# Kernel optimization log

Measured on AMD Instinct MI355X. Metric: run time of the kernel, lower is better.

The kernel has to match this reference:

```python
import jax, jax.numpy as jnp
import numpy as np

N_NODES = 50000
N_EDGES = 1600000
HID = 128
N_LAYERS = 4
EPS = 1e-5
NEG_SLOPE = 0.2


def setup_inputs() -> dict:
    key = jax.random.key(0)
    ks = jax.random.split(key, 10)
    x = jax.random.normal(ks[0], (N_NODES, HID), dtype=jnp.float32)
    edge_index = jax.random.randint(ks[1], (2, N_EDGES), 0, N_NODES, dtype=jnp.int64)
    edge_label_index = jax.random.randint(ks[2], (2, 8192), 0, N_NODES, dtype=jnp.int64)
    s = 1.0 / np.sqrt(HID)
    Wl = jax.random.uniform(ks[3], (N_LAYERS, HID, HID), jnp.float32, -s, s)
    Wr = jax.random.uniform(ks[4], (N_LAYERS, HID, HID), jnp.float32, -s, s)
    att = jax.random.uniform(ks[5], (N_LAYERS, HID), jnp.float32, -s, s)
    bias = jnp.zeros((N_LAYERS, HID), jnp.float32)
    gamma = jnp.ones((N_LAYERS, HID), jnp.float32)
    beta = jnp.zeros((N_LAYERS, HID), jnp.float32)
    return {"x": x, "edge_index": edge_index, "edge_label_index": edge_label_index,
            "Wl": Wl, "Wr": Wr, "att": att, "bias": bias, "gamma": gamma, "beta": beta}


def _gatv2_layer(x, Wl, Wr, a, b, src, dst):
    # GATv2Conv, single head: e_ij = a^T LeakyReLU(W_l x_j + W_r x_i)
    xl = x @ Wl                       # [N, H] source transform (also the message)
    xr = x @ Wr                       # [N, H] target transform
    e = jax.nn.leaky_relu(xl[src] + xr[dst], NEG_SLOPE) @ a   # [E]
    emax = jax.ops.segment_max(e, dst, num_segments=N_NODES)  # per-target max
    ew = jnp.exp(e - emax[dst])
    denom = jax.ops.segment_sum(ew, dst, num_segments=N_NODES)
    alpha = ew / denom[dst]
    out = jax.ops.segment_sum(alpha[:, None] * xl[src], dst, num_segments=N_NODES)
    return out + b


def _batchnorm(x, g, b):
    mu = jnp.mean(x, axis=0)
    var = jnp.mean(jnp.square(x - mu), axis=0)  # biased var (training mode)
    return (x - mu) * jax.lax.rsqrt(var + EPS) * g + b


def _embedding(x, edge_index, Wl, Wr, att, bias, gamma, beta):
    loops = jnp.arange(N_NODES, dtype=edge_index.dtype)
    src = jnp.concatenate([edge_index[0], loops])
    dst = jnp.concatenate([edge_index[1], loops])
    resw = 1.0 / (N_LAYERS + 1)  # alpha buffer, all entries equal
    h = x
    out = None
    for i in range(N_LAYERS):
        h = _gatv2_layer(h, Wl[i], Wr[i], att[i], bias[i], src, dst)
        h = _batchnorm(h, gamma[i], beta[i])
        out = h * resw if out is None else out + h * resw
    return out


def reference(x, edge_index, edge_label_index, Wl, Wr, att, bias, gamma, beta):
    out = _embedding(x, edge_index, Wl, Wr, att, bias, gamma, beta)
    return (out[edge_label_index[0]] * out[edge_label_index[1]]).sum(axis=-1)
```

## Files before the change

### kernel.cpp

```cpp
#include <hip/hip_runtime.h>
#include <hip/hip_bf16.h>
#include <hip/hip_fp16.h>

#define N_NODES 50000
#define N_EDGES 1600000
#define ET (N_EDGES + N_NODES)
#define HID 128
#define N_LAYERS 4
#define EPS 1e-5f
#define NEG 0.2f
#define RB 256
#define NBUCK 782
#define BCHUNK 8192
#define LOG2E 1.44269504088896f

typedef __attribute__((ext_vector_type(8))) short s16x8;
typedef __attribute__((ext_vector_type(8))) __bf16 bfx8;
typedef __attribute__((ext_vector_type(4))) float fx4;
typedef __attribute__((ext_vector_type(2))) _Float16 f16x2;

__device__ __forceinline__ unsigned int packbf2(float a, float b) {
    unsigned int ua = __float_as_uint(a);
    ua = (ua + 0x7fffu + ((ua >> 16) & 1u)) >> 16;
    unsigned int ub = __float_as_uint(b);
    ub = (ub + 0x7fffu + ((ub >> 16) & 1u)) & 0xffff0000u;
    return (ua & 0xffffu) | ub;
}
__device__ __forceinline__ unsigned short bf16r(float a) {
    unsigned int ua = __float_as_uint(a);
    return (unsigned short)((ua + 0x7fffu + ((ua >> 16) & 1u)) >> 16);
}
__device__ __forceinline__ unsigned int packh2(float a, float b) {
    return __builtin_bit_cast(unsigned int, __builtin_amdgcn_cvt_pkrtz(a, b));
}
__device__ __forceinline__ f16x2 packh2v(float a, float b) {
    return __builtin_bit_cast(f16x2, __builtin_amdgcn_cvt_pkrtz(a, b));
}
__device__ __forceinline__ float2 unpackh2(unsigned int u) {
    f16x2 h = __builtin_bit_cast(f16x2, u);
    return make_float2((float)h.x, (float)h.y);
}

__global__ void bucket_zero_kernel(int* __restrict__ gcnt) {
    int i = blockIdx.x * 256 + threadIdx.x;
    if (i < NBUCK) gcnt[i] = 0;
}

__global__ __launch_bounds__(256) void bucket_hist_kernel(const int* __restrict__ ei,
                                                          int* __restrict__ gcnt) {
    __shared__ int h[NBUCK];
    for (int i = threadIdx.x; i < NBUCK; i += 256) h[i] = 0;
    __syncthreads();
    int base = blockIdx.x * BCHUNK;
    int lim = min(base + BCHUNK, ET);
    for (int i = base + threadIdx.x; i < lim; i += 256) {
        int dst = (i < N_EDGES) ? ei[N_EDGES + i] : i - N_EDGES;
        atomicAdd(&h[dst >> 6], 1);
    }
    __syncthreads();
    for (int i = threadIdx.x; i < NBUCK; i += 256)
        if (h[i]) atomicAdd(&gcnt[i], h[i]);
}

__global__ void bucket_scan_kernel(const int* __restrict__ gcnt, int* __restrict__ bbase,
                                   int* __restrict__ bcur, int* __restrict__ rowptr) {
    __shared__ int sh[1024];
    int tid = threadIdx.x;
    int v = (tid < NBUCK) ? gcnt[tid] : 0;
    sh[tid] = v;
    __syncthreads();
    for (int off = 1; off < 1024; off <<= 1) {
        int t = (tid >= off) ? sh[tid - off] : 0;
        __syncthreads();
        sh[tid] += t;
        __syncthreads();
    }
    if (tid < NBUCK) {
        int ex = sh[tid] - v;
        bbase[tid] = ex;
        bcur[tid] = ex;
    }
    if (tid == NBUCK - 1) bbase[NBUCK] = sh[tid];
    if (tid == 0) rowptr[N_NODES] = ET;
}

__global__ __launch_bounds__(256) void bucket_scatter_kernel(const int* __restrict__ ei,
                                                             int* __restrict__ bcur,
                                                             unsigned int* __restrict__ pairs) {
    __shared__ int h[NBUCK];
    __shared__ int rbase[NBUCK];
    for (int i = threadIdx.x; i < NBUCK; i += 256) h[i] = 0;
    __syncthreads();
    int base = blockIdx.x * BCHUNK;
    int lim = min(base + BCHUNK, ET);
    for (int i = base + threadIdx.x; i < lim; i += 256) {
        int dst = (i < N_EDGES) ? ei[N_EDGES + i] : i - N_EDGES;
        atomicAdd(&h[dst >> 6], 1);
    }
    __syncthreads();
    for (int i = threadIdx.x; i < NBUCK; i += 256) {
        rbase[i] = h[i] ? atomicAdd(&bcur[i], h[i]) : 0;
        h[i] = 0;
    }
    __syncthreads();
    for (int i = base + threadIdx.x; i < lim; i += 256) {
        int src, dst;
        if (i < N_EDGES) { src = ei[i]; dst = ei[N_EDGES + i]; }
        else { src = dst = i - N_EDGES; }
        int b = dst >> 6;
        int pos = rbase[b] + atomicAdd(&h[b], 1);
        pairs[pos] = (unsigned int)src | ((unsigned int)(dst & 63) << 16);
    }
}

__global__ __launch_bounds__(256) void bucket_sort_kernel(const unsigned int* __restrict__ pairs,
                                                          const int* __restrict__ bbase,
                                                          int* __restrict__ rowptr,
                                                          int* __restrict__ csr_src) {
    __shared__ int h[64], ex[64], cur[64];
    int b = blockIdx.x;
    int tid = threadIdx.x;
    if (tid < 64) h[tid] = 0;
    __syncthreads();
    int bs = bbase[b], be = bbase[b + 1];
    for (int i = bs + tid; i < be; i += 256) atomicAdd(&h[pairs[i] >> 16], 1);
    __syncthreads();
    if (tid == 0) {
        int run = 0;
        for (int k = 0; k < 64; k++) { ex[k] = run; cur[k] = run; run += h[k]; }
    }
    __syncthreads();
    int n0 = b * 64;
    if (tid < 64 && n0 + tid < N_NODES) rowptr[n0 + tid] = bs + ex[tid];
    for (int i = bs + tid; i < be; i += 256) {
        unsigned int u = pairs[i];
        int ln = u >> 16;
        int pos = bs + atomicAdd(&cur[ln], 1);
        csr_src[pos] = (int)(u & 0xffffu);
    }
}

__global__ __launch_bounds__(256) void wconv_kernel(const float* __restrict__ Wl,
                                                    const float* __restrict__ Wr,
                                                    unsigned short* __restrict__ wt) {
    int m = blockIdx.x;
    const float* __restrict__ W = ((m & 1) ? Wr : Wl) + (size_t)(m >> 1) * HID * HID;
    unsigned short* __restrict__ o = wt + (size_t)m * HID * HID;
    for (int i = threadIdx.x; i < HID * HID; i += 256) {
        int k = i >> 7, c = i & 127;
        o[c * HID + k] = bf16r(W[i]);
    }
}

__global__ __launch_bounds__(256) void gemm_mfma_kernel(
    const float* __restrict__ hin_f, const unsigned int* __restrict__ hin_h,
    const unsigned short* __restrict__ wt_layer,
    unsigned int* __restrict__ xlh, unsigned int* __restrict__ xrh,
    const float* __restrict__ scale, const float* __restrict__ shift,
    unsigned int* __restrict__ accb, int donorm, int accmode) {
    __shared__ unsigned int Ash[128 * 64];
    __shared__ unsigned int Wsh[128 * 64];
    int row0 = blockIdx.x * 128;
    int tid = threadIdx.x;
    for (int i = tid; i < 2048; i += 256) {
        int r = i >> 4, ch = i & 15;
        int gr = row0 + r;
        uint4 pk = make_uint4(0u, 0u, 0u, 0u);
        if (gr < N_NODES) {
            float4 va, vb;
            if (hin_h) {
                uint4 u = ((const uint4*)(hin_h + (size_t)gr * 64))[ch];
                float2 f0 = unpackh2(u.x), f1 = unpackh2(u.y);
                float2 f2 = unpackh2(u.z), f3 = unpackh2(u.w);
                va = make_float4(f0.x, f0.y, f1.x, f1.y);
                vb = make_float4(f2.x, f2.y, f3.x, f3.y);
            } else {
                const float4* src = (const float4*)(hin_f + (size_t)gr * HID + ch * 8);
                va = src[0]; vb = src[1];
            }
            if (donorm) {
                const float4* s4 = (const float4*)(scale + ch * 8);
                const float4* t4 = (const float4*)(shift + ch * 8);
                float4 s0 = s4[0], s1 = s4[1], t0 = t4[0], t1 = t4[1];
                va.x = va.x * s0.x + t0.x; va.y = va.y * s0.y + t0.y;
                va.z = va.z * s0.z + t0.z; va.w = va.w * s0.w + t0.w;
                vb.x = vb.x * s1.x + t1.x; vb.y = vb.y * s1.y + t1.y;
                vb.z = vb.z * s1.z + t1.z; vb.w = vb.w * s1.w + t1.w;
            }
            if (accmode && blockIdx.y == 0) {
                uint4* ap = (uint4*)(accb + (size_t)gr * 64) + ch;
                uint4 av;
                if (accmode == 1) {
                    av.x = packh2(0.2f * va.x, 0.2f * va.y);
                    av.y = packh2(0.2f * va.z, 0.2f * va.w);
                    av.z = packh2(0.2f * vb.x, 0.2f * vb.y);
                    av.w = packh2(0.2f * vb.z, 0.2f * vb.w);
                } else {
                    uint4 old = *ap;
                    float2 o0 = unpackh2(old.x), o1 = unpackh2(old.y);
                    float2 o2 = unpackh2(old.z), o3 = unpackh2(old.w);
                    av.x = packh2(o0.x + 0.2f * va.x, o0.y + 0.2f * va.y);
                    av.y = packh2(o1.x + 0.2f * va.z, o1.y + 0.2f * va.w);
                    av.z = packh2(o2.x + 0.2f * vb.x, o2.y + 0.2f * vb.y);
                    av.w = packh2(o3.x + 0.2f * vb.z, o3.y + 0.2f * vb.w);
                }
                *ap = av;
            }
            pk.x = packbf2(va.x, va.y); pk.y = packbf2(va.z, va.w);
            pk.z = packbf2(vb.x, vb.y); pk.w = packbf2(vb.z, vb.w);
        }
        *(uint4*)(&Ash[r * 64 + ((ch ^ (r & 7)) << 2)]) = pk;
    }
    {
        const uint4* wm4 = (const uint4*)(wt_layer + (size_t)blockIdx.y * HID * HID);
        for (int i = tid; i < 2048; i += 256) {
            int c = i >> 4, ch = i & 15;
            uint4 v = wm4[i];
            *(uint4*)(&Wsh[c * 64 + ((ch ^ (c & 7)) << 2)]) = v;
        }
    }
    __syncthreads();

    int l = tid & 63, w = tid >> 6;
    int lr = l & 15, lk = l >> 4;
    fx4 acc0[8], acc1[8];
#pragma unroll
    for (int ct = 0; ct < 8; ct++) {
        acc0[ct] = (fx4){0.f, 0.f, 0.f, 0.f};
        acc1[ct] = (fx4){0.f, 0.f, 0.f, 0.f};
    }
#pragma unroll
    for (int kt = 0; kt < 4; kt++) {
        int ch = kt * 4 + lk;
        int n0 = w * 32 + lr, n1 = n0 + 16;
        bfx8 b0 = __builtin_bit_cast(bfx8, *(const s16x8*)(&Ash[n0 * 64 + ((ch ^ (n0 & 7)) << 2)]));
        bfx8 b1 = __builtin_bit_cast(bfx8, *(const s16x8*)(&Ash[n1 * 64 + ((ch ^ (n1 & 7)) << 2)]));
#pragma unroll
        for (int ct = 0; ct < 8; ct++) {
            int c = ct * 16 + lr;
            bfx8 aw = __builtin_bit_cast(bfx8, *(const s16x8*)(&Wsh[c * 64 + ((ch ^ (c & 7)) << 2)]));
            acc0[ct] = __builtin_amdgcn_mfma_f32_16x16x32_bf16(aw, b0, acc0[ct], 0, 0, 0);
            acc1[ct] = __builtin_amdgcn_mfma_f32_16x16x32_bf16(aw, b1, acc1[ct], 0, 0, 0);
        }
    }
    unsigned int* o = blockIdx.y ? xrh : xlh;
    int g0 = row0 + w * 32 + lr, g1 = g0 + 16;
#pragma unroll
    for (int ct = 0; ct < 8; ct++) {
        int cb = ct * 8 + lk * 2;
        if (g0 < N_NODES) {
            uint2 p0;
            p0.x = packh2(acc0[ct][0], acc0[ct][1]);
            p0.y = packh2(acc0[ct][2], acc0[ct][3]);
            *(uint2*)(o + (size_t)g0 * 64 + cb) = p0;
        }
        if (g1 < N_NODES) {
            uint2 p1;
            p1.x = packh2(acc1[ct][0], acc1[ct][1]);
            p1.y = packh2(acc1[ct][2], acc1[ct][3]);
            *(uint2*)(o + (size_t)g1 * 64 + cb) = p1;
        }
    }
}

__global__ __launch_bounds__(256) void aggregate_kernel(
    const unsigned int* __restrict__ xlh, const unsigned int* __restrict__ xrh,
    const float* __restrict__ att, const float* __restrict__ bias,
    const int* __restrict__ rowptr, const int* __restrict__ csr_src,
    unsigned int* __restrict__ hout) {
    int node = blockIdx.x * 8 + (threadIdx.x >> 5);
    if (node >= N_NODES) return;
    int hl = threadIdx.x & 31;
    int c0 = hl * 4;
    float4 a4 = *(const float4*)(att + c0);
    f16x2 alo = packh2v(a4.x * LOG2E, a4.y * LOG2E);
    f16x2 ahi = packh2v(a4.z * LOG2E, a4.w * LOG2E);
    const uint2 ru = *(const uint2*)(xrh + (size_t)node * 64 + hl * 2);
    f16x2 rlo = __builtin_bit_cast(f16x2, ru.x);
    f16x2 rhi = __builtin_bit_cast(f16x2, ru.y);
    const f16x2 negc = {(_Float16)NEG, (_Float16)NEG};
    int beg = rowptr[node], end = rowptr[node + 1];
    float m = -INFINITY, s = 0.f;
    float4 acc = make_float4(0.f, 0.f, 0.f, 0.f);
    for (int base = beg; base < end; base += 8) {
        int nn = end - base;
        if (nn > 8) nn = 8;
        int idx8 = csr_src[min(base + (hl & 7), end - 1)];
        uint2 v[8];
        float p[8];
#pragma unroll
        for (int j = 0; j < 8; j++) {
            int sj = __shfl(idx8, j, 32);
            v[j] = *(const uint2*)(xlh + (size_t)sj * 64 + hl * 2);
            f16x2 vlo = __builtin_bit_cast(f16x2, v[j].x);
            f16x2 vhi = __builtin_bit_cast(f16x2, v[j].y);
            f16x2 slo = vlo + rlo, shi = vhi + rhi;
            f16x2 mlo = __builtin_elementwise_max(slo, slo * negc);
            f16x2 mhi = __builtin_elementwise_max(shi, shi * negc);
            p[j] = __builtin_amdgcn_fdot2(mlo, alo,
                     __builtin_amdgcn_fdot2(mhi, ahi, 0.f, false), false);
        }
#pragma unroll
        for (int off = 1; off <= 16; off <<= 1) {
#pragma unroll
            for (int j = 0; j < 8; j++) p[j] += __shfl_xor(p[j], off, 32);
        }
#pragma unroll
        for (int j = 0; j < 8; j++)
            if (j >= nn) p[j] = -INFINITY;
        float pmax = fmaxf(fmaxf(fmaxf(p[0], p[1]), fmaxf(p[2], p[3])),
                           fmaxf(fmaxf(p[4], p[5]), fmaxf(p[6], p[7])));
        if (pmax > m + 8.f) {
            float c = exp2f(m - pmax);
            s *= c;
            acc.x *= c; acc.y *= c; acc.z *= c; acc.w *= c;
            m = pmax;
        }
#pragma unroll
        for (int j = 0; j < 8; j++) {
            float w = exp2f(p[j] - m);
            s += w;
            f16x2 vlo = __builtin_bit_cast(f16x2, v[j].x);
            f16x2 vhi = __builtin_bit_cast(f16x2, v[j].y);
            acc.x += w * (float)vlo.x; acc.y += w * (float)vlo.y;
            acc.z += w * (float)vhi.x; acc.w += w * (float)vhi.y;
        }
    }
    float inv = 1.f / s;
    const float4 b4 = *(const float4*)(bias + c0);
    uint2 po;
    po.x = packh2(acc.x * inv + b4.x, acc.y * inv + b4.y);
    po.y = packh2(acc.z * inv + b4.z, acc.w * inv + b4.w);
    *(uint2*)(hout + (size_t)node * 64 + hl * 2) = po;
}

__global__ __launch_bounds__(256) void bn_reduce_kernel(const unsigned int* __restrict__ h,
                                                        float* __restrict__ part) {
    int tid = threadIdx.x;
    int cu = tid & 63, half = tid >> 6;
    float s0 = 0.f, q0 = 0.f, s1 = 0.f, q1 = 0.f;
    for (int r = blockIdx.x * 4 + half; r < N_NODES; r += RB * 4) {
        float2 v = unpackh2(h[(size_t)r * 64 + cu]);
        s0 += v.x; q0 += v.x * v.x;
        s1 += v.y; q1 += v.y * v.y;
    }
    __shared__ float sh[256];
    sh[half * 64 + cu] = s0;
    __syncthreads();
    if (tid < 64) {
        float r0 = sh[tid] + sh[64 + tid] + sh[128 + tid] + sh[192 + tid];
        part[blockIdx.x * 256 + tid * 2] = r0;
    }
    __syncthreads();
    sh[half * 64 + cu] = q0;
    __syncthreads();
    if (tid < 64) {
        float r0 = sh[tid] + sh[64 + tid] + sh[128 + tid] + sh[192 + tid];
        part[blockIdx.x * 256 + 128 + tid * 2] = r0;
    }
    __syncthreads();
    sh[half * 64 + cu] = s1;
    __syncthreads();
    if (tid < 64) {
        float r0 = sh[tid] + sh[64 + tid] + sh[128 + tid] + sh[192 + tid];
        part[blockIdx.x * 256 + tid * 2 + 1] = r0;
    }
    __syncthreads();
    sh[half * 64 + cu] = q1;
    __syncthreads();
    if (tid < 64) {
        float r0 = sh[tid] + sh[64 + tid] + sh[128 + tid] + sh[192 + tid];
        part[blockIdx.x * 256 + 128 + tid * 2 + 1] = r0;
    }
}

__global__ void bn_finalize_kernel(const float* __restrict__ part,
                                   const float* __restrict__ gamma,
                                   const float* __restrict__ beta,
                                   float* __restrict__ scale, float* __restrict__ shift) {
    int c = threadIdx.x;
    float s = 0.f, q = 0.f;
    for (int b = 0; b < RB; b++) {
        s += part[b * 256 + c];
        q += part[b * 256 + 128 + c];
    }
    float m = s / (float)N_NODES;
    float v = q / (float)N_NODES - m * m;
    if (v < 0.f) v = 0.f;
    float rs = rsqrtf(v + EPS);
    float sc = rs * gamma[c];
    scale[c] = sc;
    shift[c] = beta[c] - m * sc;
}

__global__ __launch_bounds__(256) void accb_kernel(const unsigned int* __restrict__ h,
                                                   const float* __restrict__ scale,
                                                   const float* __restrict__ shift,
                                                   unsigned int* __restrict__ acc) {
    int idx = blockIdx.x * 256 + threadIdx.x;
    if (idx >= N_NODES * 64) return;
    int c = (idx & 63) * 2;
    float2 v = unpackh2(h[idx]);
    float n0 = v.x * scale[c] + shift[c];
    float n1 = v.y * scale[c + 1] + shift[c + 1];
    float2 a = unpackh2(acc[idx]);
    acc[idx] = packh2(a.x + 0.2f * n0, a.y + 0.2f * n1);
}

__global__ __launch_bounds__(256) void predict_kernel(const unsigned int* __restrict__ acc,
                                                      const int* __restrict__ eli,
                                                      float* __restrict__ out) {
    int p = blockIdx.x * 4 + (threadIdx.x >> 6);
    if (p >= 8192) return;
    int lane = threadIdx.x & 63;
    int i = eli[p], j = eli[8192 + p];
    f16x2 va = __builtin_bit_cast(f16x2, acc[(size_t)i * 64 + lane]);
    f16x2 vb = __builtin_bit_cast(f16x2, acc[(size_t)j * 64 + lane]);
    float t = (float)va.x * (float)vb.x + (float)va.y * (float)vb.y;
#pragma unroll
    for (int off = 32; off; off >>= 1) t += __shfl_xor(t, off, 64);
    if (lane == 0) out[p] = t;
}

extern "C" void kernel_launch(void* const* d_in, const int* in_sizes, int n_in,
                              void* d_out, int out_size, void* d_ws, size_t ws_size,
                              hipStream_t stream) {
    const float* x = (const float*)d_in[0];
    const int* ei = (const int*)d_in[1];
    const int* eli = (const int*)d_in[2];
    const float* Wl = (const float*)d_in[3];
    const float* Wr = (const float*)d_in[4];
    const float* att = (const float*)d_in[5];
    const float* bias = (const float*)d_in[6];
    const float* gamma = (const float*)d_in[7];
    const float* beta = (const float*)d_in[8];
    float* out = (float*)d_out;

    char* ws = (char*)d_ws;
    size_t off = 0;
    unsigned int* hbuf = (unsigned int*)(ws + off); off += (size_t)N_NODES * HID * 2;
    unsigned int* accb = (unsigned int*)(ws + off); off += (size_t)N_NODES * HID * 2;
    unsigned int* xlh  = (unsigned int*)(ws + off); off += (size_t)N_NODES * HID * 2;
    unsigned int* xrh  = (unsigned int*)(ws + off); off += (size_t)N_NODES * HID * 2;
    int* rowptr = (int*)(ws + off);   off += ((size_t)(N_NODES + 1) * 4 + 31) & ~31ul;
    int* csr_src = (int*)(ws + off);  off += (size_t)(ET + 8) * 4;
    int* gcnt  = (int*)(ws + off);    off += (size_t)NBUCK * 4;
    int* bcur  = (int*)(ws + off);    off += (size_t)NBUCK * 4;
    int* bbase = (int*)(ws + off);    off += (size_t)(NBUCK + 1) * 4;
    float* part = (float*)(ws + off); off += (size_t)RB * 256 * 4;
    float* scale = (float*)(ws + off); off += 128 * 4;
    float* shift = (float*)(ws + off); off += 128 * 4;
    unsigned short* wt = (unsigned short*)(ws + off); off += (size_t)8 * HID * HID * 2;
    unsigned int* pairs = (unsigned int*)(ws + off); off += (size_t)ET * 4;

    wconv_kernel<<<8, 256, 0, stream>>>(Wl, Wr, wt);

    int nablk = (ET + BCHUNK - 1) / BCHUNK;
    bucket_zero_kernel<<<(NBUCK + 255) / 256, 256, 0, stream>>>(gcnt);
    bucket_hist_kernel<<<nablk, 256, 0, stream>>>(ei, gcnt);
    bucket_scan_kernel<<<1, 1024, 0, stream>>>(gcnt, bbase, bcur, rowptr);
    bucket_scatter_kernel<<<nablk, 256, 0, stream>>>(ei, bcur, pairs);
    bucket_sort_kernel<<<NBUCK, 256, 0, stream>>>(pairs, bbase, rowptr, csr_src);

    for (int l = 0; l < N_LAYERS; l++) {
        int donorm = (l == 0) ? 0 : 1;
        int accmode = (l == 0) ? 0 : (l == 1 ? 1 : 2);
        gemm_mfma_kernel<<<dim3((N_NODES + 127) / 128, 2), 256, 0, stream>>>(
            (l == 0) ? x : nullptr, (l == 0) ? nullptr : hbuf,
            wt + (size_t)l * 2 * HID * HID, xlh, xrh, scale, shift, accb,
            donorm, accmode);
        aggregate_kernel<<<(N_NODES + 7) / 8, 256, 0, stream>>>(
            xlh, xrh, att + l * HID, bias + l * HID, rowptr, csr_src, hbuf);
        bn_reduce_kernel<<<RB, 256, 0, stream>>>(hbuf, part);
        bn_finalize_kernel<<<1, 128, 0, stream>>>(part, gamma + l * HID, beta + l * HID,
                                                  scale, shift);
    }
    accb_kernel<<<(N_NODES * 64 + 255) / 256, 256, 0, stream>>>(hbuf, scale, shift, accb);
    predict_kernel<<<8192 / 4, 256, 0, stream>>>(accb, eli, out);
}
```

Baseline: 596.4 us.

## Drop online softmax max, use 16-bit CSR indices, merge Wl/Wr GEMM blocks

The aggregate kernel stops tracking a running max for the softmax. It uses a transpose-style shuffle reduction so each lane computes one edge's score and exponent, then broadcasts the weights. Column indices are stored as 16-bit values, which halves index traffic. The GEMM now computes both Wl and Wr per block, so the input tile is loaded and normalized once instead of twice. Skipping the max subtraction risks exp overflow for large attention scores, and 16-bit indices only hold because node ids fit in 16 bits (N_NODES=50000).

Result: slower. 609.5 us (+2.2%).

```diff
diff --git a/kernel.cpp b/kernel.cpp
--- a/kernel.cpp
+++ b/kernel.cpp
@@ -116,7 +116,7 @@
 __global__ __launch_bounds__(256) void bucket_sort_kernel(const unsigned int* __restrict__ pairs,
                                                           const int* __restrict__ bbase,
                                                           int* __restrict__ rowptr,
-                                                          int* __restrict__ csr_src) {
+                                                          unsigned short* __restrict__ csr_src) {
     __shared__ int h[64], ex[64], cur[64];
     int b = blockIdx.x;
     int tid = threadIdx.x;
@@ -136,7 +136,7 @@
         unsigned int u = pairs[i];
         int ln = u >> 16;
         int pos = bs + atomicAdd(&cur[ln], 1);
-        csr_src[pos] = (int)(u & 0xffffu);
+        csr_src[pos] = (unsigned short)(u & 0xffffu);
     }
 }
 
@@ -187,7 +187,7 @@
                 vb.x = vb.x * s1.x + t1.x; vb.y = vb.y * s1.y + t1.y;
                 vb.z = vb.z * s1.z + t1.z; vb.w = vb.w * s1.w + t1.w;
             }
-            if (accmode && blockIdx.y == 0) {
+            if (accmode) {
                 uint4* ap = (uint4*)(accb + (size_t)gr * 64) + ch;
                 uint4 av;
                 if (accmode == 1) {
@@ -211,54 +211,57 @@
         }
         *(uint4*)(&Ash[r * 64 + ((ch ^ (r & 7)) << 2)]) = pk;
     }
-    {
-        const uint4* wm4 = (const uint4*)(wt_layer + (size_t)blockIdx.y * HID * HID);
+
+    int l = tid & 63, w = tid >> 6;
+    int lr = l & 15, lk = l >> 4;
+
+    for (int mat = 0; mat < 2; mat++) {
+        const uint4* wm4 = (const uint4*)(wt_layer + (size_t)mat * HID * HID);
+        if (mat) __syncthreads();
         for (int i = tid; i < 2048; i += 256) {
             int c = i >> 4, ch = i & 15;
             uint4 v = wm4[i];
             *(uint4*)(&Wsh[c * 64 + ((ch ^ (c & 7)) << 2)]) = v;
         }
-    }
-    __syncthreads();
-
-    int l = tid & 63, w = tid >> 6;
-    int lr = l & 15, lk = l >> 4;
-    fx4 acc0[8], acc1[8];
-#pragma unroll
-    for (int ct = 0; ct < 8; ct++) {
-        acc0[ct] = (fx4){0.f, 0.f, 0.f, 0.f};
-        acc1[ct] = (fx4){0.f, 0.f, 0.f, 0.f};
-    }
-#pragma unroll
-    for (int kt = 0; kt < 4; kt++) {
-        int ch = kt * 4 + lk;
-        int n0 = w * 32 + lr, n1 = n0 + 16;
-        bfx8 b0 = __builtin_bit_cast(bfx8, *(const s16x8*)(&Ash[n0 * 64 + ((ch ^ (n0 & 7)) << 2)]));
-        bfx8 b1 = __builtin_bit_cast(bfx8, *(const s16x8*)(&Ash[n1 * 64 + ((ch ^ (n1 & 7)) << 2)]));
+        __syncthreads();
+
+        fx4 acc0[8], acc1[8];
 #pragma unroll
         for (int ct = 0; ct < 8; ct++) {
-            int c = ct * 16 + lr;
-            bfx8 aw = __builtin_bit_cast(bfx8, *(const s16x8*)(&Wsh[c * 64 + ((ch ^ (c & 7)) << 2)]));
-            acc0[ct] = __builtin_amdgcn_mfma_f32_16x16x32_bf16(aw, b0, acc0[ct], 0, 0, 0);
-            acc1[ct] = __builtin_amdgcn_mfma_f32_16x16x32_bf16(aw, b1, acc1[ct], 0, 0, 0);
-        }
-    }
-    unsigned int* o = blockIdx.y ? xrh : xlh;
-    int g0 = row0 + w * 32 + lr, g1 = g0 + 16;
-#pragma unroll
-    for (int ct = 0; ct < 8; ct++) {
-        int cb = ct * 8 + lk * 2;
-        if (g0 < N_NODES) {
-            uint2 p0;
-            p0.x = packh2(acc0[ct][0], acc0[ct][1]);
-            p0.y = packh2(acc0[ct][2], acc0[ct][3]);
-            *(uint2*)(o + (size_t)g0 * 64 + cb) = p0;
-        }
-        if (g1 < N_NODES) {
-            uint2 p1;
-            p1.x = packh2(acc1[ct][0], acc1[ct][1]);
-            p1.y = packh2(acc1[ct][2], acc1[ct][3]);
-            *(uint2*)(o + (size_t)g1 * 64 + cb) = p1;
+            acc0[ct] = (fx4){0.f, 0.f, 0.f, 0.f};
+            acc1[ct] = (fx4){0.f, 0.f, 0.f, 0.f};
+        }
+#pragma unroll
+        for (int kt = 0; kt < 4; kt++) {
+            int ch = kt * 4 + lk;
+            int n0 = w * 32 + lr, n1 = n0 + 16;
+            bfx8 b0 = __builtin_bit_cast(bfx8, *(const s16x8*)(&Ash[n0 * 64 + ((ch ^ (n0 & 7)) << 2)]));
+            bfx8 b1 = __builtin_bit_cast(bfx8, *(const s16x8*)(&Ash[n1 * 64 + ((ch ^ (n1 & 7)) << 2)]));
+#pragma unroll
+            for (int ct = 0; ct < 8; ct++) {
+                int c = ct * 16 + lr;
+                bfx8 aw = __builtin_bit_cast(bfx8, *(const s16x8*)(&Wsh[c * 64 + ((ch ^ (c & 7)) << 2)]));
+                acc0[ct] = __builtin_amdgcn_mfma_f32_16x16x32_bf16(aw, b0, acc0[ct], 0, 0, 0);
+                acc1[ct] = __builtin_amdgcn_mfma_f32_16x16x32_bf16(aw, b1, acc1[ct], 0, 0, 0);
+            }
+        }
+        unsigned int* o = mat ? xrh : xlh;
+        int g0 = row0 + w * 32 + lr, g1 = g0 + 16;
+#pragma unroll
+        for (int ct = 0; ct < 8; ct++) {
+            int cb = ct * 8 + lk * 2;
+            if (g0 < N_NODES) {
+                uint2 p0;
+                p0.x = packh2(acc0[ct][0], acc0[ct][1]);
+                p0.y = packh2(acc0[ct][2], acc0[ct][3]);
+                *(uint2*)(o + (size_t)g0 * 64 + cb) = p0;
+            }
+            if (g1 < N_NODES) {
+                uint2 p1;
+                p1.x = packh2(acc1[ct][0], acc1[ct][1]);
+                p1.y = packh2(acc1[ct][2], acc1[ct][3]);
+                *(uint2*)(o + (size_t)g1 * 64 + cb) = p1;
+            }
         }
     }
 }
@@ -266,7 +269,7 @@
 __global__ __launch_bounds__(256) void aggregate_kernel(
     const unsigned int* __restrict__ xlh, const unsigned int* __restrict__ xrh,
     const float* __restrict__ att, const float* __restrict__ bias,
-    const int* __restrict__ rowptr, const int* __restrict__ csr_src,
+    const int* __restrict__ rowptr, const unsigned short* __restrict__ csr_src,
     unsigned int* __restrict__ hout) {
     int node = blockIdx.x * 8 + (threadIdx.x >> 5);
     if (node >= N_NODES) return;
@@ -280,12 +283,14 @@
     f16x2 rhi = __builtin_bit_cast(f16x2, ru.y);
     const f16x2 negc = {(_Float16)NEG, (_Float16)NEG};
     int beg = rowptr[node], end = rowptr[node + 1];
-    float m = -INFINITY, s = 0.f;
+    bool b0 = (hl & 1) != 0, b1 = (hl & 2) != 0, b2 = (hl & 4) != 0;
+    int myj = hl & 7;
+    float s = 0.f;
     float4 acc = make_float4(0.f, 0.f, 0.f, 0.f);
     for (int base = beg; base < end; base += 8) {
         int nn = end - base;
         if (nn > 8) nn = 8;
-        int idx8 = csr_src[min(base + (hl & 7), end - 1)];
+        int idx8 = (int)csr_src[min(base + myj, end - 1)];
         uint2 v[8];
         float p[8];
 #pragma unroll
@@ -300,30 +305,24 @@
             p[j] = __builtin_amdgcn_fdot2(mlo, alo,
                      __builtin_amdgcn_fdot2(mhi, ahi, 0.f, false), false);
         }
-#pragma unroll
-        for (int off = 1; off <= 16; off <<= 1) {
-#pragma unroll
-            for (int j = 0; j < 8; j++) p[j] += __shfl_xor(p[j], off, 32);
-        }
-#pragma unroll
-        for (int j = 0; j < 8; j++)
-            if (j >= nn) p[j] = -INFINITY;
-        float pmax = fmaxf(fmaxf(fmaxf(p[0], p[1]), fmaxf(p[2], p[3])),
-                           fmaxf(fmaxf(p[4], p[5]), fmaxf(p[6], p[7])));
-        if (pmax > m + 8.f) {
-            float c = exp2f(m - pmax);
-            s *= c;
-            acc.x *= c; acc.y *= c; acc.z *= c; acc.w *= c;
-            m = pmax;
-        }
+        float q0 = (b0 ? p[1] : p[0]) + __shfl_xor(b0 ? p[0] : p[1], 1, 32);
+        float q1 = (b0 ? p[3] : p[2]) + __shfl_xor(b0 ? p[2] : p[3], 1, 32);
+        float q2 = (b0 ? p[5] : p[4]) + __shfl_xor(b0 ? p[4] : p[5], 1, 32);
+        float q3 = (b0 ? p[7] : p[6]) + __shfl_xor(b0 ? p[6] : p[7], 1, 32);
+        float r0 = (b1 ? q1 : q0) + __shfl_xor(b1 ? q0 : q1, 2, 32);
+        float r1 = (b1 ? q3 : q2) + __shfl_xor(b1 ? q2 : q3, 2, 32);
+        float f  = (b2 ? r1 : r0) + __shfl_xor(b2 ? r0 : r1, 4, 32);
+        f += __shfl_xor(f, 8, 32);
+        f += __shfl_xor(f, 16, 32);
+        float wown = (myj < nn) ? exp2f(f) : 0.f;
 #pragma unroll
         for (int j = 0; j < 8; j++) {
-            float w = exp2f(p[j] - m);
-            s += w;
+            float wj = __shfl(wown, j, 8);
+            s += wj;
             f16x2 vlo = __builtin_bit_cast(f16x2, v[j].x);
             f16x2 vhi = __builtin_bit_cast(f16x2, v[j].y);
-            acc.x += w * (float)vlo.x; acc.y += w * (float)vlo.y;
-            acc.z += w * (float)vhi.x; acc.w += w * (float)vhi.y;
+            acc.x += wj * (float)vlo.x; acc.y += wj * (float)vlo.y;
+            acc.z += wj * (float)vhi.x; acc.w += wj * (float)vhi.y;
         }
     }
     float inv = 1.f / s;
@@ -443,7 +442,7 @@
     unsigned int* xlh  = (unsigned int*)(ws + off); off += (size_t)N_NODES * HID * 2;
     unsigned int* xrh  = (unsigned int*)(ws + off); off += (size_t)N_NODES * HID * 2;
     int* rowptr = (int*)(ws + off);   off += ((size_t)(N_NODES + 1) * 4 + 31) & ~31ul;
-    int* csr_src = (int*)(ws + off);  off += (size_t)(ET + 8) * 4;
+    unsigned short* csr_src = (unsigned short*)(ws + off); off += ((size_t)(ET + 16) * 2 + 31) & ~31ul;
     int* gcnt  = (int*)(ws + off);    off += (size_t)NBUCK * 4;
     int* bcur  = (int*)(ws + off);    off += (size_t)NBUCK * 4;
     int* bbase = (int*)(ws + off);    off += (size_t)(NBUCK + 1) * 4;
@@ -465,7 +464,7 @@
     for (int l = 0; l < N_LAYERS; l++) {
         int donorm = (l == 0) ? 0 : 1;
         int accmode = (l == 0) ? 0 : (l == 1 ? 1 : 2);
-        gemm_mfma_kernel<<<dim3((N_NODES + 127) / 128, 2), 256, 0, stream>>>(
+        gemm_mfma_kernel<<<(N_NODES + 127) / 128, 256, 0, stream>>>(
             (l == 0) ? x : nullptr, (l == 0) ? nullptr : hbuf,
             wt + (size_t)l * 2 * HID * HID, xlh, xrh, scale, shift, accb,
             donorm, accmode);
```
